# Kernel tuning notes

Hardware: AMD Instinct MI355X
Metric: run time of the kernel (lower is better)

Reference implementation:

```python
import jax, jax.numpy as jnp
import numpy as np

B, TN, TE = 64, 131072, 262144
QD, ND, ED, P = 768, 512, 512, 512


def setup_inputs() -> dict:
    key = jax.random.key(0)
    ks = jax.random.split(key, 20)
    s = 0.02  # weight init scale
    return {
        "question": jax.random.normal(ks[0], (B, QD), jnp.float32),
        "nodes": jax.random.normal(ks[1], (TN, ND), jnp.float32),
        "edges": jax.random.normal(ks[2], (TE, ED), jnp.float32),
        "W_nq": jax.random.normal(ks[3], (QD, P), jnp.float32) * s,
        "b_nq": jnp.zeros((P,), jnp.float32),
        "W_n": jax.random.normal(ks[4], (ND, P), jnp.float32) * s,
        "b_n": jnp.zeros((P,), jnp.float32),
        "w_nv": jax.random.normal(ks[5], (P,), jnp.float32) * s,
        "b_nv": jnp.zeros((), jnp.float32),
        "W_eq": jax.random.normal(ks[6], (QD, P), jnp.float32) * s,
        "b_eq": jnp.zeros((P,), jnp.float32),
        "W_e": jax.random.normal(ks[7], (ED, P), jnp.float32) * s,
        "b_e": jnp.zeros((P,), jnp.float32),
        "w_ev": jax.random.normal(ks[8], (P,), jnp.float32) * s,
        "b_ev": jnp.zeros((), jnp.float32),
        "node_gid": jnp.sort(jax.random.randint(ks[9], (TN,), 0, B, jnp.int32)),
        "edge_gid": jnp.sort(jax.random.randint(ks[10], (TE,), 0, B, jnp.int32)),
    }


def segment_softmax(scores, seg_ids, num_segments):
    # numerically stable softmax within each graph's segment
    m = jax.ops.segment_max(scores, seg_ids, num_segments=num_segments)
    e = jnp.exp(scores - m[seg_ids])
    z = jax.ops.segment_sum(e, seg_ids, num_segments=num_segments)
    return e / z[seg_ids]


def reference(question, nodes, edges, W_nq, b_nq, W_n, b_n, w_nv, b_nv,
              W_eq, b_eq, W_e, b_e, w_ev, b_ev, node_gid, edge_gid):
    # question-conditioned projections, broadcast to each graph's elements
    qn = question @ W_nq + b_nq                      # [B, P]
    qe = question @ W_eq + b_eq                      # [B, P]
    hn = nodes @ W_n + b_n                           # [TN, P]
    he = edges @ W_e + b_e                           # [TE, P]
    s_n = jnp.tanh(hn + qn[node_gid]) @ w_nv + b_nv  # [TN]
    s_e = jnp.tanh(he + qe[edge_gid]) @ w_ev + b_ev  # [TE]
    att_n = segment_softmax(s_n, node_gid, B)        # per-graph softmax over nodes
    att_e = segment_softmax(s_e, edge_gid, B)        # per-graph softmax over edges
    return att_n, att_e
```

## Files before the change

kernel.cpp:

```cpp
#include <hip/hip_runtime.h>
#include <hip/hip_bf16.h>


typedef __attribute__((ext_vector_type(4))) float  floatx4;
typedef __attribute__((ext_vector_type(8))) short  shortx8;

#define TN_CONST 131072
#define TE_CONST 262144
#define BM 64
#define BK 32
#define NSTEP 16

__device__ __forceinline__ unsigned short f2bf(float f) {
    union { float f; unsigned u; } v; v.f = f;
    unsigned u = v.u;
    unsigned r = (u + 0x7FFFu + ((u >> 16) & 1u)) >> 16;
    return (unsigned short)r;
}

__device__ __forceinline__ void gload16(const void* g, void* l) {
    __builtin_amdgcn_global_load_lds((const __attribute__((address_space(1))) void*)g,
                                     (__attribute__((address_space(3))) void*)l,
                                     16, 0, 0);
}

__global__ void prep_wt_kernel(const float* __restrict__ Wn, const float* __restrict__ We,
                               unsigned short* __restrict__ Wtn, unsigned short* __restrict__ Wte)
{
    int c = blockIdx.x * 256 + threadIdx.x;
    const int sel = c >> 18;
    const int idx = c & 262143;
    const int p = idx >> 9, k = idx & 511;
    const float* W = sel ? We : Wn;
    unsigned short* Wt = sel ? Wte : Wtn;
    Wt[((k >> 5) << 14) + (p << 5) + (k & 31)] = f2bf(W[(size_t)k * 512 + p]);
}

__global__ void prep_q_kernel(const float* __restrict__ question,
                              const float* __restrict__ Wnq, const float* __restrict__ bnq,
                              const float* __restrict__ bn,
                              const float* __restrict__ Weq, const float* __restrict__ beq,
                              const float* __restrict__ be,
                              float* __restrict__ Qpn, float* __restrict__ Qpe)
{
    const int b     = blockIdx.x;
    const int which = blockIdx.y;
    const int kc    = blockIdx.z;
    const int p     = threadIdx.x;
    const float* W  = which ? Weq : Wnq;
    const float* bq = which ? beq : bnq;
    const float* bh = which ? be  : bn;
    float* Qp       = which ? Qpe : Qpn;
    const float* q  = question + b * 768;
    float s = 0.f;
    const int kbeg = kc * 192, kend = kbeg + 192;
    for (int k = kbeg; k < kend; ++k) s += q[k] * W[(size_t)k * 512 + p];
    if (kc == 0) s += bq[p] + bh[p];
    atomicAdd(&Qp[b * 512 + p], s);
}

__global__ __launch_bounds__(512, 1)
void fused_gemm_attn(const float* __restrict__ A,
                     const unsigned short* __restrict__ Bt,
                     const float* __restrict__ Qp,
                     const float* __restrict__ wv,
                     const float* __restrict__ bvp,
                     const int*   __restrict__ gid,
                     float* __restrict__ eout,
                     float* __restrict__ zglob)
{
    __shared__ float          As32[4][BM][BK];
    __shared__ unsigned short Bs[2][512][BK];
    __shared__ float sred[4][BM];
    __shared__ float zpart[64];
    __shared__ int   gsh[64];

    const int tid  = threadIdx.x;
    const int wave = tid >> 6;
    const int lane = tid & 63;
    const int m16  = lane & 15;
    const int q4   = lane >> 4;
    const int wr   = wave >> 2;
    const int wc   = wave & 3;
    const long r0  = (long)blockIdx.x * BM;

    if (tid < 64) { gsh[tid] = gid[r0 + tid]; zpart[tid] = 0.f; }

    const int arow = tid >> 3;
    const int achk = tid & 7;
    const float* asrc = A + (size_t)(r0 + arow) * 512 + ((achk ^ (arow & 7)) << 2);
    const unsigned short* bsrc = Bt + (size_t)tid * 8;

    floatx4 acc[2][8];
#pragma unroll
    for (int i = 0; i < 2; ++i)
#pragma unroll
        for (int j = 0; j < 8; ++j) acc[i][j] = (floatx4){0.f, 0.f, 0.f, 0.f};

#pragma unroll
    for (int i = 0; i < 4; ++i)
        gload16(bsrc + i * 4096, (char*)&Bs[0][0][0] + (tid + i * 512) * 16);
    gload16(asrc,      (char*)&As32[0][0][0] + tid * 16);
    gload16(asrc + 32, (char*)&As32[1][0][0] + tid * 16);

#pragma unroll
    for (int t = 0; t < NSTEP; ++t) {
        if (t + 1 < NSTEP) {
#pragma unroll
            for (int i = 0; i < 4; ++i)
                gload16(bsrc + (size_t)(t + 1) * 16384 + i * 4096,
                        (char*)&Bs[(t + 1) & 1][0][0] + (tid + i * 512) * 16);
        }
        if (t + 2 < NSTEP)
            gload16(asrc + (t + 2) * BK, (char*)&As32[(t + 2) & 3][0][0] + tid * 16);

        if (t < NSTEP - 2)       asm volatile("s_waitcnt vmcnt(6)" ::: "memory");
        else if (t == NSTEP - 2) asm volatile("s_waitcnt vmcnt(5)" ::: "memory");
        else                     asm volatile("s_waitcnt vmcnt(0)" ::: "memory");
        __builtin_amdgcn_s_barrier();

        shortx8 af[2];
#pragma unroll
        for (int i = 0; i < 2; ++i) {
            const int row = wr * 32 + i * 16 + m16;
            const float* ap = &As32[t & 3][row][0];
            const float4 lo = *(const float4*)(ap + (((q4 * 2 + 0) ^ (m16 & 7)) << 2));
            const float4 hi = *(const float4*)(ap + (((q4 * 2 + 1) ^ (m16 & 7)) << 2));
            shortx8 r;
            r[0] = (short)f2bf(lo.x); r[1] = (short)f2bf(lo.y);
            r[2] = (short)f2bf(lo.z); r[3] = (short)f2bf(lo.w);
            r[4] = (short)f2bf(hi.x); r[5] = (short)f2bf(hi.y);
            r[6] = (short)f2bf(hi.z); r[7] = (short)f2bf(hi.w);
            af[i] = r;
        }
#pragma unroll
        for (int j = 0; j < 8; ++j) {
            const shortx8 bfr = *(const shortx8*)&Bs[t & 1][wc * 128 + j * 16 + m16][q4 * 8];
#pragma unroll
            for (int i = 0; i < 2; ++i)
                acc[i][j] = __builtin_amdgcn_mfma_f32_16x16x32_bf16(af[i], bfr, acc[i][j], 0, 0, 0);
        }
        __builtin_amdgcn_s_barrier();
    }

    const float bv = bvp[0];
    float wvp[8];
#pragma unroll
    for (int j = 0; j < 8; ++j) wvp[j] = wv[wc * 128 + j * 16 + m16];

#pragma unroll
    for (int i = 0; i < 2; ++i) {
#pragma unroll
        for (int reg = 0; reg < 4; ++reg) {
            const int row = wr * 32 + i * 16 + q4 * 4 + reg;
            const int g   = gsh[row];
            const float* qrow = Qp + (size_t)g * 512 + wc * 128 + m16;
            float partial = 0.f;
#pragma unroll
            for (int j = 0; j < 8; ++j) {
                float h  = acc[i][j][reg] + qrow[j * 16];
                float ex = __expf(2.f * h);
                float tt = (ex - 1.f) * __builtin_amdgcn_rcpf(ex + 1.f);
                partial += tt * wvp[j];
            }
            partial += __shfl_xor(partial, 1);
            partial += __shfl_xor(partial, 2);
            partial += __shfl_xor(partial, 4);
            partial += __shfl_xor(partial, 8);
            if (m16 == 0) sred[wc][row] = partial;
        }
    }
    __syncthreads();
    if (tid < BM) {
        float s = bv + sred[0][tid] + sred[1][tid] + sred[2][tid] + sred[3][tid];
        float e = __expf(s);
        eout[r0 + tid] = e;
        atomicAdd(&zpart[gsh[tid]], e);
    }
    __syncthreads();
    if (tid < 64) {
        float v = zpart[tid];
        if (v != 0.f) atomicAdd(&zglob[tid], v);
    }
}

__global__ void norm_kernel(float* __restrict__ out, const int* __restrict__ ngid,
                            const int* __restrict__ egid, const float* __restrict__ z)
{
    int idx = blockIdx.x * 256 + threadIdx.x;
    float zz;
    if (idx < TN_CONST) zz = z[ngid[idx]];
    else                zz = z[64 + egid[idx - TN_CONST]];
    out[idx] = out[idx] / zz;
}

extern "C" void kernel_launch(void* const* d_in, const int* in_sizes, int n_in,
                              void* d_out, int out_size, void* d_ws, size_t ws_size,
                              hipStream_t stream)
{
    const float* question = (const float*)d_in[0];
    const float* nodes    = (const float*)d_in[1];
    const float* edges    = (const float*)d_in[2];
    const float* W_nq     = (const float*)d_in[3];
    const float* b_nq     = (const float*)d_in[4];
    const float* W_n      = (const float*)d_in[5];
    const float* b_n      = (const float*)d_in[6];
    const float* w_nv     = (const float*)d_in[7];
    const float* b_nv     = (const float*)d_in[8];
    const float* W_eq     = (const float*)d_in[9];
    const float* b_eq     = (const float*)d_in[10];
    const float* W_e      = (const float*)d_in[11];
    const float* b_e      = (const float*)d_in[12];
    const float* w_ev     = (const float*)d_in[13];
    const float* b_ev     = (const float*)d_in[14];
    const int* node_gid   = (const int*)d_in[15];
    const int* edge_gid   = (const int*)d_in[16];
    float* out = (float*)d_out;

    char* ws = (char*)d_ws;
    float*          z   = (float*)(ws);
    float*          Qpn = (float*)(ws + 512);
    float*          Qpe = (float*)(ws + 131584);
    unsigned short* Wtn = (unsigned short*)(ws + 262656);
    unsigned short* Wte = (unsigned short*)(ws + 786944);

    hipMemsetAsync(ws, 0, 262656, stream);

    prep_wt_kernel<<<2048, 256, 0, stream>>>(W_n, W_e, Wtn, Wte);
    prep_q_kernel<<<dim3(64, 2, 4), 512, 0, stream>>>(question, W_nq, b_nq, b_n,
                                                      W_eq, b_eq, b_e, Qpn, Qpe);
    fused_gemm_attn<<<TN_CONST / BM, 512, 0, stream>>>(nodes, Wtn, Qpn, w_nv, b_nv,
                                                       node_gid, out, z);
    fused_gemm_attn<<<TE_CONST / BM, 512, 0, stream>>>(edges, Wte, Qpe, w_ev, b_ev,
                                                       edge_gid, out + TN_CONST, z + 64);
    norm_kernel<<<1536, 256, 0, stream>>>(out, node_gid, edge_gid, z);
}
```

Before: 1.264 ms.

## Load A fragments straight to registers and triple-buffer B in LDS

Drops the LDS staging of the fp32 A tile. Each lane now loads its MFMA A fragment directly from global memory into registers, double-buffered two steps ahead. B tiles move to a three-stage LDS ring with prefetch distance two, which removes the second barrier per k-step. Float-to-bf16 conversion switches to a perm-based pack that rounds half-up instead of round-to-nearest-even. The aim is less LDS traffic, fewer barriers and cheaper conversion, at the cost of more registers, uncoalesced per-lane global A loads, and slightly different rounding.

```diff
diff --git a/kernel.cpp b/kernel.cpp
--- a/kernel.cpp
+++ b/kernel.cpp
@@ -16,6 +16,11 @@
     unsigned u = v.u;
     unsigned r = (u + 0x7FFFu + ((u >> 16) & 1u)) >> 16;
     return (unsigned short)r;
+}
+
+__device__ __forceinline__ unsigned packbf(float lo, float hi) {
+    union { float f; unsigned u; } a, b; a.f = lo; b.f = hi;
+    return __builtin_amdgcn_perm(b.u + 0x8000u, a.u + 0x8000u, 0x07060302u);
 }
 
 __device__ __forceinline__ void gload16(const void* g, void* l) {
@@ -69,8 +74,7 @@
                      float* __restrict__ eout,
                      float* __restrict__ zglob)
 {
-    __shared__ float          As32[4][BM][BK];
-    __shared__ unsigned short Bs[2][512][BK];
+    __shared__ unsigned short Bs[3][512][BK];
     __shared__ float sred[4][BM];
     __shared__ float zpart[64];
     __shared__ int   gsh[64];
@@ -85,62 +89,72 @@
     const long r0  = (long)blockIdx.x * BM;
 
     if (tid < 64) { gsh[tid] = gid[r0 + tid]; zpart[tid] = 0.f; }
-
-    const int arow = tid >> 3;
-    const int achk = tid & 7;
-    const float* asrc = A + (size_t)(r0 + arow) * 512 + ((achk ^ (arow & 7)) << 2);
+    __builtin_amdgcn_sched_barrier(0);
+
     const unsigned short* bsrc = Bt + (size_t)tid * 8;
+    const float* aptr0 = A + (size_t)(r0 + wr * 32 + m16) * 512 + q4 * 8;
+    const float* aptr1 = aptr0 + 16 * 512;
 
     floatx4 acc[2][8];
 #pragma unroll
     for (int i = 0; i < 2; ++i)
 #pragma unroll
         for (int j = 0; j < 8; ++j) acc[i][j] = (floatx4){0.f, 0.f, 0.f, 0.f};
+
+    float4 apf[2][4];
 
 #pragma unroll
     for (int i = 0; i < 4; ++i)
         gload16(bsrc + i * 4096, (char*)&Bs[0][0][0] + (tid + i * 512) * 16);
-    gload16(asrc,      (char*)&As32[0][0][0] + tid * 16);
-    gload16(asrc + 32, (char*)&As32[1][0][0] + tid * 16);
+    apf[0][0] = *(const float4*)(aptr0);
+    apf[0][1] = *(const float4*)(aptr0 + 4);
+    apf[0][2] = *(const float4*)(aptr1);
+    apf[0][3] = *(const float4*)(aptr1 + 4);
+#pragma unroll
+    for (int i = 0; i < 4; ++i)
+        gload16(bsrc + 16384 + i * 4096, (char*)&Bs[1][0][0] + (tid + i * 512) * 16);
+    apf[1][0] = *(const float4*)(aptr0 + 32);
+    apf[1][1] = *(const float4*)(aptr0 + 36);
+    apf[1][2] = *(const float4*)(aptr1 + 32);
+    apf[1][3] = *(const float4*)(aptr1 + 36);
 
 #pragma unroll
     for (int t = 0; t < NSTEP; ++t) {
-        if (t + 1 < NSTEP) {
+        if (t < NSTEP - 1) asm volatile("s_waitcnt vmcnt(8)" ::: "memory");
+        else               asm volatile("s_waitcnt vmcnt(0)" ::: "memory");
+        __builtin_amdgcn_s_barrier();
+
+        shortx8 af[2];
+#pragma unroll
+        for (int i = 0; i < 2; ++i) {
+            const float4 lo = apf[t & 1][i * 2];
+            const float4 hi = apf[t & 1][i * 2 + 1];
+            union { shortx8 v; unsigned u[4]; } r;
+            r.u[0] = packbf(lo.x, lo.y);
+            r.u[1] = packbf(lo.z, lo.w);
+            r.u[2] = packbf(hi.x, hi.y);
+            r.u[3] = packbf(hi.z, hi.w);
+            af[i] = r.v;
+        }
+
+        if (t + 2 < NSTEP) {
 #pragma unroll
             for (int i = 0; i < 4; ++i)
-                gload16(bsrc + (size_t)(t + 1) * 16384 + i * 4096,
-                        (char*)&Bs[(t + 1) & 1][0][0] + (tid + i * 512) * 16);
-        }
-        if (t + 2 < NSTEP)
-            gload16(asrc + (t + 2) * BK, (char*)&As32[(t + 2) & 3][0][0] + tid * 16);
-
-        if (t < NSTEP - 2)       asm volatile("s_waitcnt vmcnt(6)" ::: "memory");
-        else if (t == NSTEP - 2) asm volatile("s_waitcnt vmcnt(5)" ::: "memory");
-        else                     asm volatile("s_waitcnt vmcnt(0)" ::: "memory");
-        __builtin_amdgcn_s_barrier();
-
-        shortx8 af[2];
-#pragma unroll
-        for (int i = 0; i < 2; ++i) {
-            const int row = wr * 32 + i * 16 + m16;
-            const float* ap = &As32[t & 3][row][0];
-            const float4 lo = *(const float4*)(ap + (((q4 * 2 + 0) ^ (m16 & 7)) << 2));
-            const float4 hi = *(const float4*)(ap + (((q4 * 2 + 1) ^ (m16 & 7)) << 2));
-            shortx8 r;
-            r[0] = (short)f2bf(lo.x); r[1] = (short)f2bf(lo.y);
-            r[2] = (short)f2bf(lo.z); r[3] = (short)f2bf(lo.w);
-            r[4] = (short)f2bf(hi.x); r[5] = (short)f2bf(hi.y);
-            r[6] = (short)f2bf(hi.z); r[7] = (short)f2bf(hi.w);
-            af[i] = r;
-        }
+                gload16(bsrc + (size_t)(t + 2) * 16384 + i * 4096,
+                        (char*)&Bs[(t + 2) % 3][0][0] + (tid + i * 512) * 16);
+            apf[t & 1][0] = *(const float4*)(aptr0 + (t + 2) * 32);
+            apf[t & 1][1] = *(const float4*)(aptr0 + (t + 2) * 32 + 4);
+            apf[t & 1][2] = *(const float4*)(aptr1 + (t + 2) * 32);
+            apf[t & 1][3] = *(const float4*)(aptr1 + (t + 2) * 32 + 4);
+        }
+
 #pragma unroll
         for (int j = 0; j < 8; ++j) {
-            const shortx8 bfr = *(const shortx8*)&Bs[t & 1][wc * 128 + j * 16 + m16][q4 * 8];
+            const shortx8 bfr = *(const shortx8*)&Bs[t % 3][wc * 128 + j * 16 + m16][q4 * 8];
 #pragma unroll
             for (int i = 0; i < 2; ++i)
                 acc[i][j] = __builtin_amdgcn_mfma_f32_16x16x32_bf16(af[i], bfr, acc[i][j], 0, 0, 0);
         }
-        __builtin_amdgcn_s_barrier();
     }
 
     const float bv = bvp[0];
```

After: 1.466 ms. 1.16x slower.
